# Kernel optimization log

Hardware: AMD Instinct MI355X
Metric: run time of the kernel (lower is better)

The kernel has to match this reference:

```python
import jax, jax.numpy as jnp
import numpy as np

B, N, D_V, D_H, D_K = 1024, 131072, 256, 256, 256


def setup_inputs() -> dict:
    key = jax.random.key(0)
    ks = jax.random.split(key, 12)
    s = 0.02
    V = jax.random.normal(ks[0], (B, D_V), dtype=jnp.float32)
    H = jax.random.normal(ks[1], (N, D_H), dtype=jnp.float32)
    batch_idx = jnp.sort(jax.random.randint(ks[2], (N,), 0, B)).astype(jnp.int32)
    Wq = jax.random.normal(ks[3], (D_K, D_V), dtype=jnp.float32) / np.sqrt(D_V)
    bq = jnp.zeros((D_K,), dtype=jnp.float32)
    Wk = jax.random.normal(ks[4], (D_K, D_H), dtype=jnp.float32) / np.sqrt(D_H)
    bk = jnp.zeros((D_K,), dtype=jnp.float32)
    Wv = jax.random.normal(ks[5], (D_V, D_H), dtype=jnp.float32) / np.sqrt(D_H)
    bv = jnp.zeros((D_V,), dtype=jnp.float32)
    Wo = jax.random.normal(ks[6], (D_V, 2 * D_V), dtype=jnp.float32) / np.sqrt(2 * D_V)
    bo = jnp.zeros((D_V,), dtype=jnp.float32)
    return {"V": V, "H": H, "batch_idx": batch_idx,
            "Wq": Wq, "bq": bq, "Wk": Wk, "bk": bk,
            "Wv": Wv, "bv": bv, "Wo": Wo, "bo": bo}


def reference(V, H, batch_idx, Wq, bq, Wk, bk, Wv, bv, Wo, bo):
    nb = V.shape[0]
    Q = V @ Wq.T + bq            # [B, d_k] one query per graph
    K = H @ Wk.T + bk            # [N, d_k]
    Vval = H @ Wv.T + bv         # [N, d_v]
    scale = 1.0 / jnp.sqrt(jnp.asarray(K.shape[-1], K.dtype))
    # ragged attention scores: each node attends to its graph's query
    scores = jnp.einsum('nd,nd->n', K, Q[batch_idx]) * scale   # [N]
    m = jax.ops.segment_max(scores, batch_idx, num_segments=nb)  # [B]
    e = jnp.exp(scores - m[batch_idx])
    denom = jax.ops.segment_sum(e, batch_idx, num_segments=nb)   # [B]
    attn = e / denom[batch_idx]                                  # [N]
    H_tilde = jax.ops.segment_sum(attn[:, None] * Vval, batch_idx, num_segments=nb)  # [B, d_v]
    U = jnp.concatenate([V, H_tilde], axis=-1)                   # [B, 2*d_v]
    out = U @ Wo.T + bo                                          # [B, d_v]
    # graphs with zero nodes pass V through unchanged
    count = jax.ops.segment_sum(jnp.ones_like(scores), batch_idx, num_segments=nb)
    return jnp.where((count > 0)[:, None], out, V)
```

## Files before the change

kernel.cpp:

```cpp
#include <hip/hip_runtime.h>
#include <math.h>

#define D 256
#define TWOD 512
#define BB 1024
#define NN 131072
#define LOG2E 1.4426950408889634f

typedef float v4f __attribute__((ext_vector_type(4)));

__device__ __forceinline__ v4f ldg_nt(const float* p, bool valid) {
  v4f z = {0.f, 0.f, 0.f, 0.f};
  if (valid) z = __builtin_nontemporal_load((const v4f*)p);
  return z;
}

__device__ __forceinline__ float dot4(v4f a, v4f b) {
  return fmaf(a.w, b.w, fmaf(a.z, b.z, fmaf(a.y, b.y, a.x * b.x)));
}

__device__ __forceinline__ float pack4(float d0, float d1, float d2, float d3) {
  float a01 = d0 + __shfl_xor(d1, 4);
  float a23 = d2 + __shfl_xor(d3, 4);
  float s = a01 + __shfl_xor(a23, 8);
  s += __shfl_xor(s, 1);
  s += __shfl_xor(s, 2);
  s += __shfl_xor(s, 16);
  s += __shfl_xor(s, 32);
  return s;
}

__global__ __launch_bounds__(256) void a_kernel(
    const float* __restrict__ V, const float* __restrict__ Wq,
    const float* __restrict__ Wk, const float* __restrict__ bq,
    const float* __restrict__ Wv, const float* __restrict__ Wo,
    const int* __restrict__ bidx,
    float* __restrict__ qt, float* __restrict__ WvT,
    float* __restrict__ WoT, int* __restrict__ offs) {
  __shared__ __align__(16) char smem[24576];
  const int blk = blockIdx.x;
  const int t = threadIdx.x;

  if (blk < 256) {
    float* Vs   = (float*)smem;
    float* q1s4 = (float*)(smem + 4096);
    float* part = (float*)(smem + 8192);
    const int wq = t >> 6, lane = t & 63;
    const int b0 = blk * 4;
    for (int i = 0; i < 4; ++i) Vs[i * 256 + t] = V[(size_t)(b0 + i) * D + t];
    __syncthreads();
    const int rot = (lane >> 2) & 3;
    const v4f vb0 = *(const v4f*)&Vs[0 * 256 + lane * 4];
    const v4f vb1 = *(const v4f*)&Vs[1 * 256 + lane * 4];
    const v4f vb2 = *(const v4f*)&Vs[2 * 256 + lane * 4];
    const v4f vb3 = *(const v4f*)&Vs[3 * 256 + lane * 4];

    for (int ii = 0; ii < 16; ++ii) {
      const int cb = wq * 64 + ii * 4;
      const v4f r0 = *(const v4f*)(Wq + (size_t)(cb + (rot ^ 0)) * D + lane * 4);
      const v4f r1 = *(const v4f*)(Wq + (size_t)(cb + (rot ^ 1)) * D + lane * 4);
      const v4f r2 = *(const v4f*)(Wq + (size_t)(cb + (rot ^ 2)) * D + lane * 4);
      const v4f r3 = *(const v4f*)(Wq + (size_t)(cb + (rot ^ 3)) * D + lane * 4);
      const float s0 = pack4(dot4(r0, vb0), dot4(r1, vb0), dot4(r2, vb0), dot4(r3, vb0));
      const float s1 = pack4(dot4(r0, vb1), dot4(r1, vb1), dot4(r2, vb1), dot4(r3, vb1));
      const float s2 = pack4(dot4(r0, vb2), dot4(r1, vb2), dot4(r2, vb2), dot4(r3, vb2));
      const float s3 = pack4(dot4(r0, vb3), dot4(r1, vb3), dot4(r2, vb3), dot4(r3, vb3));
      if (lane < 16 && (lane & 3) == 0) {
        v4f o = {s0, s1, s2, s3};
        *(v4f*)&q1s4[(cb + rot) * 4] = o;
      }
    }
    __syncthreads();

    v4f a0 = {0.f, 0.f, 0.f, 0.f}, a1 = a0, a2 = a0, a3 = a0;
    const int kb = wq * 64;
    for (int kk = 0; kk < 64; ++kk) {
      const int k = kb + kk;
      const v4f w4 = *(const v4f*)(Wk + (size_t)k * D + lane * 4);
      const v4f q = *(const v4f*)&q1s4[k * 4];
      const float bqk = bq[k];
      a0 += w4 * (q.x + bqk);
      a1 += w4 * (q.y + bqk);
      a2 += w4 * (q.z + bqk);
      a3 += w4 * (q.w + bqk);
    }
    *(v4f*)&part[(wq * 4 + 0) * 256 + lane * 4] = a0;
    *(v4f*)&part[(wq * 4 + 1) * 256 + lane * 4] = a1;
    *(v4f*)&part[(wq * 4 + 2) * 256 + lane * 4] = a2;
    *(v4f*)&part[(wq * 4 + 3) * 256 + lane * 4] = a3;
    __syncthreads();
    #pragma unroll
    for (int b = 0; b < 4; ++b) {
      const float s = part[(0 * 4 + b) * 256 + t] + part[(1 * 4 + b) * 256 + t] +
                      part[(2 * 4 + b) * 256 + t] + part[(3 * 4 + b) * 256 + t];
      qt[(size_t)(b0 + b) * D + t] = s;
    }
  } else if (blk < 304) {
    float (*tile)[65] = (float(*)[65])smem;
    const float* src; float* dst; int r0, c0, C;
    if (blk < 272) { int b = blk - 256; src = Wv; dst = WvT; C = 256; r0 = (b >> 2) * 64; c0 = (b & 3) * 64; }
    else           { int b = blk - 272; src = Wo; dst = WoT; C = 512; r0 = (b >> 3) * 64; c0 = (b & 7) * 64; }
    const int lane = t & 63, sr = t >> 6;
    #pragma unroll 4
    for (int rr = 0; rr < 16; ++rr) {
      const int r = rr * 4 + sr;
      tile[r][lane] = src[(size_t)(r0 + r) * C + c0 + lane];
    }
    __syncthreads();
    #pragma unroll 4
    for (int rr = 0; rr < 16; ++rr) {
      const int r = rr * 4 + sr;
      dst[(size_t)(c0 + r) * 256 + r0 + lane] = tile[lane][r];
    }
  } else {
    const int i = (blk - 304) * 256 + t;
    if (i >= NN) return;
    const int b1 = bidx[i];
    const int b2 = (i + 1 < NN) ? bidx[i + 1] : BB;
    if (i == 0) {
      for (int b = 0; b <= b1; ++b) offs[b] = 0;
    }
    for (int b = b1 + 1; b <= b2; ++b) offs[b] = i + 1;
  }
}

__global__ __launch_bounds__(1024) void f_kernel(
    const float* __restrict__ H, const float* __restrict__ qt,
    const int* __restrict__ offs, const float* __restrict__ V,
    const float* __restrict__ WvT, const float* __restrict__ WoT,
    const float* __restrict__ bv, const float* __restrict__ bo,
    float* __restrict__ out) {
  __shared__ __align__(16) float ss[16][D];
  __shared__ float sm[16], sd[16];
  __shared__ __align__(16) float sN2[D][4];
  __shared__ __align__(16) float Us2[TWOD][4];
  __shared__ __align__(16) float part[8][4][D];

  const int t = threadIdx.x;
  const int wave = t >> 6, lane = t & 63;
  const int blk = blockIdx.x;
  const int ib = wave >> 2, qq = wave & 3;
  const int bb = blk * 4 + ib;

  const int start = offs[bb], end = offs[bb + 1];
  const int cnt = end - start;
  const int step = (cnt + 3) >> 2;
  const int s0 = start + min(cnt, qq * step);
  const int e0 = start + min(cnt, (qq + 1) * step);

  float m = -1e30f, den = 0.f;
  v4f acc = {0.f, 0.f, 0.f, 0.f};

  if (s0 < e0) {
    const v4f q4 = *(const v4f*)(qt + (size_t)bb * D + lane * 4);
    const float SC = 0.0625f * LOG2E;
    const int odd = lane & 1;
    int n = s0;
    v4f c0 = ldg_nt(H + (size_t)n * D + lane * 4, true);
    v4f c1 = ldg_nt(H + (size_t)(n + 1) * D + lane * 4, n + 1 < e0);
    while (n < e0) {
      v4f p0 = ldg_nt(H + (size_t)(n + 2) * D + lane * 4, n + 2 < e0);
      v4f p1 = ldg_nt(H + (size_t)(n + 3) * D + lane * 4, n + 3 < e0);

      const float d0 = dot4(c0, q4);
      const float d1 = dot4(c1, q4);
      const float mine = odd ? d1 : d0;
      const float oth  = odd ? d0 : d1;
      float s = mine + __shfl_xor(oth, 1);
      s += __shfl_xor(s, 2);
      s += __shfl_xor(s, 4);
      s += __shfl_xor(s, 8);
      s += __shfl_xor(s, 16);
      s += __shfl_xor(s, 32);
      const float sc = (n + odd < e0) ? s * SC : -1e30f;

      const float mm = fmaxf(sc, __shfl_xor(sc, 1));
      const float nm = fmaxf(m, mm);
      const float f = exp2f(m - nm);
      const float w = exp2f(sc - nm);
      const float wx = __shfl_xor(w, 1);
      const float wr0 = odd ? wx : w;
      const float wr1 = odd ? w : wx;
      den = fmaf(den, f, w + wx);
      acc = acc * f + c0 * wr0 + c1 * wr1;
      m = nm;

      c0 = p0; c1 = p1; n += 2;
    }
  }
  *(v4f*)&ss[wave][lane * 4] = acc;
  if (lane == 0) { sm[wave] = m; sd[wave] = den; }
  __syncthreads();

  {
    const int i = t >> 8, d = t & 255;
    const int w0 = i * 4;
    const float m0 = sm[w0], m1 = sm[w0 + 1], m2 = sm[w0 + 2], m3 = sm[w0 + 3];
    const float M = fmaxf(fmaxf(m0, m1), fmaxf(m2, m3));
    const float f0 = exp2f(m0 - M), f1 = exp2f(m1 - M);
    const float f2 = exp2f(m2 - M), f3 = exp2f(m3 - M);
    const float Dn = sd[w0] * f0 + sd[w0 + 1] * f1 + sd[w0 + 2] * f2 + sd[w0 + 3] * f3;
    const float inv = (Dn > 0.f) ? (1.f / Dn) : 0.f;
    sN2[d][i] = (ss[w0][d] * f0 + ss[w0 + 1][d] * f1 +
                 ss[w0 + 2][d] * f2 + ss[w0 + 3][d] * f3) * inv;
    Us2[d][i] = V[(size_t)(blk * 4 + i) * D + d];
  }
  __syncthreads();

  v4f a0 = {0.f, 0.f, 0.f, 0.f}, a1 = a0, a2 = a0, a3 = a0;
  {
    const int hb = wave * 16;
    #pragma unroll 4
    for (int hh = 0; hh < 16; ++hh) {
      const int h = hb + hh;
      const v4f w4 = *(const v4f*)(WvT + (size_t)h * D + lane * 4);
      const v4f s4 = *(const v4f*)&sN2[h][0];
      a0 += w4 * s4.x; a1 += w4 * s4.y; a2 += w4 * s4.z; a3 += w4 * s4.w;
    }
  }
  if (wave >= 8) {
    *(v4f*)&part[wave - 8][0][lane * 4] = a0;
    *(v4f*)&part[wave - 8][1][lane * 4] = a1;
    *(v4f*)&part[wave - 8][2][lane * 4] = a2;
    *(v4f*)&part[wave - 8][3][lane * 4] = a3;
  }
  __syncthreads();
  if (wave < 8) {
    v4f p0 = *(const v4f*)&part[wave][0][lane * 4];
    v4f p1 = *(const v4f*)&part[wave][1][lane * 4];
    v4f p2 = *(const v4f*)&part[wave][2][lane * 4];
    v4f p3 = *(const v4f*)&part[wave][3][lane * 4];
    *(v4f*)&part[wave][0][lane * 4] = a0 + p0;
    *(v4f*)&part[wave][1][lane * 4] = a1 + p1;
    *(v4f*)&part[wave][2][lane * 4] = a2 + p2;
    *(v4f*)&part[wave][3][lane * 4] = a3 + p3;
  }
  __syncthreads();
  {
    const int i = t >> 8, d = t & 255;
    float s = bv[d];
    #pragma unroll
    for (int w = 0; w < 8; ++w) s += part[w][i][d];
    Us2[D + d][i] = s;
  }
  __syncthreads();

  a0 = (v4f){0.f, 0.f, 0.f, 0.f}; a1 = a0; a2 = a0; a3 = a0;
  {
    const int kb = wave * 32;
    #pragma unroll 4
    for (int kk = 0; kk < 32; ++kk) {
      const int k = kb + kk;
      const v4f w4 = *(const v4f*)(WoT + (size_t)k * D + lane * 4);
      const v4f u4 = *(const v4f*)&Us2[k][0];
      a0 += w4 * u4.x; a1 += w4 * u4.y; a2 += w4 * u4.z; a3 += w4 * u4.w;
    }
  }
  if (wave >= 8) {
    *(v4f*)&part[wave - 8][0][lane * 4] = a0;
    *(v4f*)&part[wave - 8][1][lane * 4] = a1;
    *(v4f*)&part[wave - 8][2][lane * 4] = a2;
    *(v4f*)&part[wave - 8][3][lane * 4] = a3;
  }
  __syncthreads();
  if (wave < 8) {
    v4f p0 = *(const v4f*)&part[wave][0][lane * 4];
    v4f p1 = *(const v4f*)&part[wave][1][lane * 4];
    v4f p2 = *(const v4f*)&part[wave][2][lane * 4];
    v4f p3 = *(const v4f*)&part[wave][3][lane * 4];
    *(v4f*)&part[wave][0][lane * 4] = a0 + p0;
    *(v4f*)&part[wave][1][lane * 4] = a1 + p1;
    *(v4f*)&part[wave][2][lane * 4] = a2 + p2;
    *(v4f*)&part[wave][3][lane * 4] = a3 + p3;
  }
  __syncthreads();
  {
    const int i = t >> 8, d = t & 255;
    const int bb2 = blk * 4 + i;
    float s = bo[d];
    #pragma unroll
    for (int w = 0; w < 8; ++w) s += part[w][i][d];
    const int c = offs[bb2 + 1] - offs[bb2];
    out[(size_t)bb2 * D + d] = (c > 0) ? s : Us2[d][i];
  }
}

extern "C" void kernel_launch(void* const* d_in, const int* in_sizes, int n_in,
                              void* d_out, int out_size, void* d_ws, size_t ws_size,
                              hipStream_t stream) {
  const float* V   = (const float*)d_in[0];
  const float* H   = (const float*)d_in[1];
  const int* bidx  = (const int*)d_in[2];
  const float* Wq  = (const float*)d_in[3];
  const float* bq  = (const float*)d_in[4];
  const float* Wk  = (const float*)d_in[5];
  const float* Wv  = (const float*)d_in[7];
  const float* bv  = (const float*)d_in[8];
  const float* Wo  = (const float*)d_in[9];
  const float* bo  = (const float*)d_in[10];
  float* out = (float*)d_out;

  float* ws  = (float*)d_ws;
  float* WvT = ws;
  float* WoT = WvT + D * D;
  float* qt  = WoT + TWOD * D;
  int* offs  = (int*)(qt + BB * D);

  hipLaunchKernelGGL(a_kernel, dim3(816), dim3(256), 0, stream,
                     V, Wq, Wk, bq, Wv, Wo, bidx, qt, WvT, WoT, offs);
  hipLaunchKernelGGL(f_kernel, dim3(BB / 4), dim3(1024), 0, stream,
                     H, qt, offs, V, WvT, WoT, bv, bo, out);
}
```

Measured before the change: 53.15 us.

## Fuse query projection into attention kernel and interleave node rows across waves

The Wq/Wk query-key projection moves out of the prologue kernel and into each attention block, so every block computes its own 4 folded query vectors in shared memory. This removes the qt global write and read and shrinks the first kernel to transposes plus offsets. Node rows are now interleaved across the four waves of a graph, in pairs with stride 8, rather than split into contiguous chunks. Shared memory is aliased between phases, which needs an extra barrier. In exchange, the f_kernel prologue is longer (it reads Wq and Wk per block), and that work now sits serially before the H streaming loop instead of in a separate kernel.

Measured after the change: 56.65 us. 1.07x slower.

```diff
diff --git a/kernel.cpp b/kernel.cpp
--- a/kernel.cpp
+++ b/kernel.cpp
@@ -30,33 +30,79 @@
   return s;
 }
 
-__global__ __launch_bounds__(256) void a_kernel(
-    const float* __restrict__ V, const float* __restrict__ Wq,
-    const float* __restrict__ Wk, const float* __restrict__ bq,
+__global__ __launch_bounds__(256) void t_kernel(
     const float* __restrict__ Wv, const float* __restrict__ Wo,
     const int* __restrict__ bidx,
-    float* __restrict__ qt, float* __restrict__ WvT,
-    float* __restrict__ WoT, int* __restrict__ offs) {
-  __shared__ __align__(16) char smem[24576];
+    float* __restrict__ WvT, float* __restrict__ WoT,
+    int* __restrict__ offs) {
   const int blk = blockIdx.x;
   const int t = threadIdx.x;
-
-  if (blk < 256) {
-    float* Vs   = (float*)smem;
-    float* q1s4 = (float*)(smem + 4096);
-    float* part = (float*)(smem + 8192);
-    const int wq = t >> 6, lane = t & 63;
-    const int b0 = blk * 4;
-    for (int i = 0; i < 4; ++i) Vs[i * 256 + t] = V[(size_t)(b0 + i) * D + t];
+  if (blk < 48) {
+    __shared__ float tile[64][65];
+    const float* src; float* dst; int r0, c0, C;
+    if (blk < 16) { src = Wv; dst = WvT; C = 256; r0 = (blk >> 2) * 64; c0 = (blk & 3) * 64; }
+    else          { int b = blk - 16; src = Wo; dst = WoT; C = 512; r0 = (b >> 3) * 64; c0 = (b & 7) * 64; }
+    const int lane = t & 63, sr = t >> 6;
+    #pragma unroll 4
+    for (int rr = 0; rr < 16; ++rr) {
+      const int r = rr * 4 + sr;
+      tile[r][lane] = src[(size_t)(r0 + r) * C + c0 + lane];
+    }
     __syncthreads();
+    #pragma unroll 4
+    for (int rr = 0; rr < 16; ++rr) {
+      const int r = rr * 4 + sr;
+      dst[(size_t)(c0 + r) * 256 + r0 + lane] = tile[lane][r];
+    }
+  } else {
+    const int i = (blk - 48) * 256 + t;
+    if (i >= NN) return;
+    const int b1 = bidx[i];
+    const int b2 = (i + 1 < NN) ? bidx[i + 1] : BB;
+    if (i == 0) {
+      for (int b = 0; b <= b1; ++b) offs[b] = 0;
+    }
+    for (int b = b1 + 1; b <= b2; ++b) offs[b] = i + 1;
+  }
+}
+
+__global__ __launch_bounds__(1024) void f_kernel(
+    const float* __restrict__ H, const float* __restrict__ V,
+    const float* __restrict__ Wq, const float* __restrict__ Wk,
+    const float* __restrict__ bq, const int* __restrict__ offs,
+    const float* __restrict__ WvT, const float* __restrict__ WoT,
+    const float* __restrict__ bv, const float* __restrict__ bo,
+    float* __restrict__ out) {
+  __shared__ __align__(16) char smem[61440];
+  float* partq = (float*)smem;
+  float (*ss)[D] = (float(*)[D])smem;
+  float* Vs   = (float*)(smem + 16384);
+  float* sN2  = (float*)(smem + 16384);
+  float* q1s4 = (float*)(smem + 20480);
+  float* Us2  = (float*)(smem + 20480);
+  float (*part)[4][D] = (float(*)[4][D])(smem + 28672);
+  __shared__ float sm[16], sd[16];
+
+  const int t = threadIdx.x;
+  const int wave = t >> 6, lane = t & 63;
+  const int blk = blockIdx.x;
+  const int b0 = blk * 4;
+
+  {
+    const int i = t >> 8, d = t & 255;
+    Vs[i * 256 + d] = V[(size_t)(b0 + i) * D + d];
+  }
+  __syncthreads();
+
+  {
     const int rot = (lane >> 2) & 3;
     const v4f vb0 = *(const v4f*)&Vs[0 * 256 + lane * 4];
     const v4f vb1 = *(const v4f*)&Vs[1 * 256 + lane * 4];
     const v4f vb2 = *(const v4f*)&Vs[2 * 256 + lane * 4];
     const v4f vb3 = *(const v4f*)&Vs[3 * 256 + lane * 4];
-
-    for (int ii = 0; ii < 16; ++ii) {
-      const int cb = wq * 64 + ii * 4;
+    #pragma unroll
+    for (int ii = 0; ii < 4; ++ii) {
+      const int cb = wave * 16 + ii * 4;
       const v4f r0 = *(const v4f*)(Wq + (size_t)(cb + (rot ^ 0)) * D + lane * 4);
       const v4f r1 = *(const v4f*)(Wq + (size_t)(cb + (rot ^ 1)) * D + lane * 4);
       const v4f r2 = *(const v4f*)(Wq + (size_t)(cb + (rot ^ 2)) * D + lane * 4);
@@ -70,97 +116,48 @@
         *(v4f*)&q1s4[(cb + rot) * 4] = o;
       }
     }
-    __syncthreads();
-
-    v4f a0 = {0.f, 0.f, 0.f, 0.f}, a1 = a0, a2 = a0, a3 = a0;
-    const int kb = wq * 64;
+  }
+  __syncthreads();
+
+  {
+    const int i = wave & 3, kq = wave >> 2;
+    v4f aq = {0.f, 0.f, 0.f, 0.f};
+    const int kb = kq * 64;
     for (int kk = 0; kk < 64; ++kk) {
       const int k = kb + kk;
       const v4f w4 = *(const v4f*)(Wk + (size_t)k * D + lane * 4);
-      const v4f q = *(const v4f*)&q1s4[k * 4];
-      const float bqk = bq[k];
-      a0 += w4 * (q.x + bqk);
-      a1 += w4 * (q.y + bqk);
-      a2 += w4 * (q.z + bqk);
-      a3 += w4 * (q.w + bqk);
-    }
-    *(v4f*)&part[(wq * 4 + 0) * 256 + lane * 4] = a0;
-    *(v4f*)&part[(wq * 4 + 1) * 256 + lane * 4] = a1;
-    *(v4f*)&part[(wq * 4 + 2) * 256 + lane * 4] = a2;
-    *(v4f*)&part[(wq * 4 + 3) * 256 + lane * 4] = a3;
-    __syncthreads();
-    #pragma unroll
-    for (int b = 0; b < 4; ++b) {
-      const float s = part[(0 * 4 + b) * 256 + t] + part[(1 * 4 + b) * 256 + t] +
-                      part[(2 * 4 + b) * 256 + t] + part[(3 * 4 + b) * 256 + t];
-      qt[(size_t)(b0 + b) * D + t] = s;
-    }
-  } else if (blk < 304) {
-    float (*tile)[65] = (float(*)[65])smem;
-    const float* src; float* dst; int r0, c0, C;
-    if (blk < 272) { int b = blk - 256; src = Wv; dst = WvT; C = 256; r0 = (b >> 2) * 64; c0 = (b & 3) * 64; }
-    else           { int b = blk - 272; src = Wo; dst = WoT; C = 512; r0 = (b >> 3) * 64; c0 = (b & 7) * 64; }
-    const int lane = t & 63, sr = t >> 6;
-    #pragma unroll 4
-    for (int rr = 0; rr < 16; ++rr) {
-      const int r = rr * 4 + sr;
-      tile[r][lane] = src[(size_t)(r0 + r) * C + c0 + lane];
-    }
-    __syncthreads();
-    #pragma unroll 4
-    for (int rr = 0; rr < 16; ++rr) {
-      const int r = rr * 4 + sr;
-      dst[(size_t)(c0 + r) * 256 + r0 + lane] = tile[lane][r];
-    }
-  } else {
-    const int i = (blk - 304) * 256 + t;
-    if (i >= NN) return;
-    const int b1 = bidx[i];
-    const int b2 = (i + 1 < NN) ? bidx[i + 1] : BB;
-    if (i == 0) {
-      for (int b = 0; b <= b1; ++b) offs[b] = 0;
-    }
-    for (int b = b1 + 1; b <= b2; ++b) offs[b] = i + 1;
-  }
-}
-
-__global__ __launch_bounds__(1024) void f_kernel(
-    const float* __restrict__ H, const float* __restrict__ qt,
-    const int* __restrict__ offs, const float* __restrict__ V,
-    const float* __restrict__ WvT, const float* __restrict__ WoT,
-    const float* __restrict__ bv, const float* __restrict__ bo,
-    float* __restrict__ out) {
-  __shared__ __align__(16) float ss[16][D];
-  __shared__ float sm[16], sd[16];
-  __shared__ __align__(16) float sN2[D][4];
-  __shared__ __align__(16) float Us2[TWOD][4];
-  __shared__ __align__(16) float part[8][4][D];
-
-  const int t = threadIdx.x;
-  const int wave = t >> 6, lane = t & 63;
-  const int blk = blockIdx.x;
+      aq += w4 * (q1s4[k * 4 + i] + bq[k]);
+    }
+    *(v4f*)&partq[(kq * 4 + i) * 256 + lane * 4] = aq;
+  }
+  __syncthreads();
+
   const int ib = wave >> 2, qq = wave & 3;
-  const int bb = blk * 4 + ib;
-
+  const int bb = b0 + ib;
   const int start = offs[bb], end = offs[bb + 1];
-  const int cnt = end - start;
-  const int step = (cnt + 3) >> 2;
-  const int s0 = start + min(cnt, qq * step);
-  const int e0 = start + min(cnt, (qq + 1) * step);
+
+  v4f q4;
+  {
+    const v4f p0 = *(const v4f*)&partq[(0 * 4 + ib) * 256 + lane * 4];
+    const v4f p1 = *(const v4f*)&partq[(1 * 4 + ib) * 256 + lane * 4];
+    const v4f p2 = *(const v4f*)&partq[(2 * 4 + ib) * 256 + lane * 4];
+    const v4f p3 = *(const v4f*)&partq[(3 * 4 + ib) * 256 + lane * 4];
+    q4 = (p0 + p1) + (p2 + p3);
+  }
+  __syncthreads();
 
   float m = -1e30f, den = 0.f;
   v4f acc = {0.f, 0.f, 0.f, 0.f};
-
-  if (s0 < e0) {
-    const v4f q4 = *(const v4f*)(qt + (size_t)bb * D + lane * 4);
+  {
     const float SC = 0.0625f * LOG2E;
     const int odd = lane & 1;
-    int n = s0;
-    v4f c0 = ldg_nt(H + (size_t)n * D + lane * 4, true);
-    v4f c1 = ldg_nt(H + (size_t)(n + 1) * D + lane * 4, n + 1 < e0);
-    while (n < e0) {
-      v4f p0 = ldg_nt(H + (size_t)(n + 2) * D + lane * 4, n + 2 < e0);
-      v4f p1 = ldg_nt(H + (size_t)(n + 3) * D + lane * 4, n + 3 < e0);
+    int n = start + qq * 2;
+    v4f c0 = ldg_nt(H + (size_t)n * D + lane * 4, n < end);
+    v4f c1 = ldg_nt(H + (size_t)(n + 1) * D + lane * 4, n + 1 < end);
+    while (n < end) {
+      const int nn = n + 8;
+      v4f p0 = ldg_nt(H + (size_t)nn * D + lane * 4, nn < end);
+      v4f p1 = ldg_nt(H + (size_t)(nn + 1) * D + lane * 4, nn + 1 < end);
 
       const float d0 = dot4(c0, q4);
       const float d1 = dot4(c1, q4);
@@ -172,7 +169,7 @@
       s += __shfl_xor(s, 8);
       s += __shfl_xor(s, 16);
       s += __shfl_xor(s, 32);
-      const float sc = (n + odd < e0) ? s * SC : -1e30f;
+      const float sc = (n + odd < end) ? s * SC : -1e30f;
 
       const float mm = fmaxf(sc, __shfl_xor(sc, 1));
       const float nm = fmaxf(m, mm);
@@ -185,7 +182,7 @@
       acc = acc * f + c0 * wr0 + c1 * wr1;
       m = nm;
 
-      c0 = p0; c1 = p1; n += 2;
+      c0 = p0; c1 = p1; n = nn;
     }
   }
   *(v4f*)&ss[wave][lane * 4] = acc;
@@ -201,9 +198,12 @@
     const float f2 = exp2f(m2 - M), f3 = exp2f(m3 - M);
     const float Dn = sd[w0] * f0 + sd[w0 + 1] * f1 + sd[w0 + 2] * f2 + sd[w0 + 3] * f3;
     const float inv = (Dn > 0.f) ? (1.f / Dn) : 0.f;
-    sN2[d][i] = (ss[w0][d] * f0 + ss[w0 + 1][d] * f1 +
-                 ss[w0 + 2][d] * f2 + ss[w0 + 3][d] * f3) * inv;
-    Us2[d][i] = V[(size_t)(blk * 4 + i) * D + d];
+    const float sv = (ss[w0][d] * f0 + ss[w0 + 1][d] * f1 +
+                      ss[w0 + 2][d] * f2 + ss[w0 + 3][d] * f3) * inv;
+    const float vv = V[(size_t)(b0 + i) * D + d];
+    __syncthreads();
+    sN2[d * 4 + i] = sv;
+    Us2[d * 4 + i] = vv;
   }
   __syncthreads();
 
@@ -214,7 +214,7 @@
     for (int hh = 0; hh < 16; ++hh) {
       const int h = hb + hh;
       const v4f w4 = *(const v4f*)(WvT + (size_t)h * D + lane * 4);
-      const v4f s4 = *(const v4f*)&sN2[h][0];
+      const v4f s4 = *(const v4f*)&sN2[h * 4];
       a0 += w4 * s4.x; a1 += w4 * s4.y; a2 += w4 * s4.z; a3 += w4 * s4.w;
     }
   }
@@ -241,7 +241,7 @@
     float s = bv[d];
     #pragma unroll
     for (int w = 0; w < 8; ++w) s += part[w][i][d];
-    Us2[D + d][i] = s;
+    Us2[(D + d) * 4 + i] = s;
   }
   __syncthreads();
 
@@ -252,7 +252,7 @@
     for (int kk = 0; kk < 32; ++kk) {
       const int k = kb + kk;
       const v4f w4 = *(const v4f*)(WoT + (size_t)k * D + lane * 4);
-      const v4f u4 = *(const v4f*)&Us2[k][0];
+      const v4f u4 = *(const v4f*)&Us2[k * 4];
       a0 += w4 * u4.x; a1 += w4 * u4.y; a2 += w4 * u4.z; a3 += w4 * u4.w;
     }
   }
@@ -276,12 +276,12 @@
   __syncthreads();
   {
     const int i = t >> 8, d = t & 255;
-    const int bb2 = blk * 4 + i;
+    const int bb2 = b0 + i;
     float s = bo[d];
     #pragma unroll
     for (int w = 0; w < 8; ++w) s += part[w][i][d];
     const int c = offs[bb2 + 1] - offs[bb2];
-    out[(size_t)bb2 * D + d] = (c > 0) ? s : Us2[d][i];
+    out[(size_t)bb2 * D + d] = (c > 0) ? s : Us2[d * 4 + i];
   }
 }
 
@@ -303,11 +303,10 @@
   float* ws  = (float*)d_ws;
   float* WvT = ws;
   float* WoT = WvT + D * D;
-  float* qt  = WoT + TWOD * D;
-  int* offs  = (int*)(qt + BB * D);
-
-  hipLaunchKernelGGL(a_kernel, dim3(816), dim3(256), 0, stream,
-                     V, Wq, Wk, bq, Wv, Wo, bidx, qt, WvT, WoT, offs);
+  int* offs  = (int*)(WoT + TWOD * D);
+
+  hipLaunchKernelGGL(t_kernel, dim3(560), dim3(256), 0, stream,
+                     Wv, Wo, bidx, WvT, WoT, offs);
   hipLaunchKernelGGL(f_kernel, dim3(BB / 4), dim3(1024), 0, stream,
-                     H, qt, offs, V, WvT, WoT, bv, bo, out);
-}
+                     H, V, Wq, Wk, bq, offs, WvT, WoT, bv, bo, out);
+}
```

## Fold Wv into Wo output projection and deepen H prefetch

Applied to the files above, without the earlier changes.

Precomputes a fused weight Wo[:,D:]·Wv and a combined bias cvec in the prep kernel, so the finalize stage runs one 512-wide matvec instead of two chained ones with their reductions and barriers. The streaming loop over H now prefetches two node pairs ahead instead of one, and per-graph offsets and V are staged in shared memory up front. Shared memory is aliased across phases to reduce the per-block footprint. The fused-weight computation adds serial 256-step loops to 64 prep blocks, which could lengthen the prep kernel.

Measured after the change: 54.07 us. No clear change (+1.7%).

```diff
diff --git a/kernel.cpp b/kernel.cpp
--- a/kernel.cpp
+++ b/kernel.cpp
@@ -30,13 +30,14 @@
   return s;
 }
 
-__global__ __launch_bounds__(256) void a_kernel(
+__global__ __launch_bounds__(256) void prep_kernel(
     const float* __restrict__ V, const float* __restrict__ Wq,
-    const float* __restrict__ Wk, const float* __restrict__ bq,
-    const float* __restrict__ Wv, const float* __restrict__ Wo,
+    const float* __restrict__ bq, const float* __restrict__ Wk,
+    const float* __restrict__ Wv, const float* __restrict__ bv,
+    const float* __restrict__ Wo, const float* __restrict__ bo,
     const int* __restrict__ bidx,
-    float* __restrict__ qt, float* __restrict__ WvT,
-    float* __restrict__ WoT, int* __restrict__ offs) {
+    float* __restrict__ qt, float* __restrict__ WfT,
+    float* __restrict__ cvec, int* __restrict__ offs) {
   __shared__ __align__(16) char smem[24576];
   const int blk = blockIdx.x;
   const int t = threadIdx.x;
@@ -95,25 +96,44 @@
                       part[(2 * 4 + b) * 256 + t] + part[(3 * 4 + b) * 256 + t];
       qt[(size_t)(b0 + b) * D + t] = s;
     }
-  } else if (blk < 304) {
+  } else if (blk < 320) {
+    const int h0 = (blk - 256) * 4;
+    float a0 = 0.f, a1 = 0.f, a2 = 0.f, a3 = 0.f;
+    for (int v = 0; v < D; ++v) {
+      const float wo = Wo[(size_t)t * TWOD + D + v];
+      const float* wvr = Wv + (size_t)v * D + h0;
+      a0 = fmaf(wvr[0], wo, a0);
+      a1 = fmaf(wvr[1], wo, a1);
+      a2 = fmaf(wvr[2], wo, a2);
+      a3 = fmaf(wvr[3], wo, a3);
+    }
+    WfT[(size_t)(D + h0 + 0) * D + t] = a0;
+    WfT[(size_t)(D + h0 + 1) * D + t] = a1;
+    WfT[(size_t)(D + h0 + 2) * D + t] = a2;
+    WfT[(size_t)(D + h0 + 3) * D + t] = a3;
+  } else if (blk < 336) {
     float (*tile)[65] = (float(*)[65])smem;
-    const float* src; float* dst; int r0, c0, C;
-    if (blk < 272) { int b = blk - 256; src = Wv; dst = WvT; C = 256; r0 = (b >> 2) * 64; c0 = (b & 3) * 64; }
-    else           { int b = blk - 272; src = Wo; dst = WoT; C = 512; r0 = (b >> 3) * 64; c0 = (b & 7) * 64; }
+    const int b = blk - 320;
+    const int r0 = (b >> 2) * 64, c0 = (b & 3) * 64;
     const int lane = t & 63, sr = t >> 6;
     #pragma unroll 4
     for (int rr = 0; rr < 16; ++rr) {
       const int r = rr * 4 + sr;
-      tile[r][lane] = src[(size_t)(r0 + r) * C + c0 + lane];
+      tile[r][lane] = Wo[(size_t)(r0 + r) * TWOD + c0 + lane];
     }
     __syncthreads();
     #pragma unroll 4
     for (int rr = 0; rr < 16; ++rr) {
       const int r = rr * 4 + sr;
-      dst[(size_t)(c0 + r) * 256 + r0 + lane] = tile[lane][r];
-    }
+      WfT[(size_t)(c0 + r) * D + r0 + lane] = tile[lane][r];
+    }
+  } else if (blk == 336) {
+    float a = bo[t];
+    for (int v = 0; v < D; ++v)
+      a = fmaf(Wo[(size_t)t * TWOD + D + v], bv[v], a);
+    cvec[t] = a;
   } else {
-    const int i = (blk - 304) * 256 + t;
+    const int i = (blk - 337) * 256 + t;
     if (i >= NN) return;
     const int b1 = bidx[i];
     const int b2 = (i + 1 < NN) ? bidx[i + 1] : BB;
@@ -125,42 +145,53 @@
 }
 
 __global__ __launch_bounds__(1024) void f_kernel(
-    const float* __restrict__ H, const float* __restrict__ qt,
-    const int* __restrict__ offs, const float* __restrict__ V,
-    const float* __restrict__ WvT, const float* __restrict__ WoT,
-    const float* __restrict__ bv, const float* __restrict__ bo,
+    const float* __restrict__ H, const float* __restrict__ V,
+    const float* __restrict__ qt, const int* __restrict__ offs,
+    const float* __restrict__ WfT, const float* __restrict__ cvec,
     float* __restrict__ out) {
-  __shared__ __align__(16) float ss[16][D];
+  __shared__ __align__(16) char smem[40960];
+  float (*ss)[D] = (float(*)[D])smem;
+  float (*part)[4][D] = (float(*)[4][D])smem;
+  float* Us2 = (float*)(smem + 32768);
   __shared__ float sm[16], sd[16];
-  __shared__ __align__(16) float sN2[D][4];
-  __shared__ __align__(16) float Us2[TWOD][4];
-  __shared__ __align__(16) float part[8][4][D];
+  __shared__ int soff[5];
 
   const int t = threadIdx.x;
   const int wave = t >> 6, lane = t & 63;
   const int blk = blockIdx.x;
-  const int ib = wave >> 2, qq = wave & 3;
-  const int bb = blk * 4 + ib;
-
-  const int start = offs[bb], end = offs[bb + 1];
-  const int cnt = end - start;
-  const int step = (cnt + 3) >> 2;
-  const int s0 = start + min(cnt, qq * step);
-  const int e0 = start + min(cnt, (qq + 1) * step);
+  const int b0 = blk * 4;
+
+  if (t < 5) soff[t] = offs[b0 + t];
+  {
+    const int i = t >> 8, d = t & 255;
+    Us2[d * 4 + i] = V[(size_t)(b0 + i) * D + d];
+  }
+  __syncthreads();
+
+  const int ib = wave >> 2, ph = wave & 3;
+  const int bb = b0 + ib;
+  const int start = soff[ib];
+  const int cnt = soff[ib + 1] - start;
+  const int ck = (cnt + 3) >> 2;
+  const int s0 = start + min(cnt, ph * ck);
+  const int e0 = start + min(cnt, (ph + 1) * ck);
+
+  const v4f q4 = *(const v4f*)(qt + (size_t)bb * D + lane * 4);
+  int n = s0;
+  v4f c0 = ldg_nt(H + (size_t)n * D + lane * 4, n < e0);
+  v4f c1 = ldg_nt(H + (size_t)(n + 1) * D + lane * 4, n + 1 < e0);
+  v4f f0 = ldg_nt(H + (size_t)(n + 2) * D + lane * 4, n + 2 < e0);
+  v4f f1 = ldg_nt(H + (size_t)(n + 3) * D + lane * 4, n + 3 < e0);
 
   float m = -1e30f, den = 0.f;
   v4f acc = {0.f, 0.f, 0.f, 0.f};
-
-  if (s0 < e0) {
-    const v4f q4 = *(const v4f*)(qt + (size_t)bb * D + lane * 4);
+  {
     const float SC = 0.0625f * LOG2E;
     const int odd = lane & 1;
-    int n = s0;
-    v4f c0 = ldg_nt(H + (size_t)n * D + lane * 4, true);
-    v4f c1 = ldg_nt(H + (size_t)(n + 1) * D + lane * 4, n + 1 < e0);
     while (n < e0) {
-      v4f p0 = ldg_nt(H + (size_t)(n + 2) * D + lane * 4, n + 2 < e0);
-      v4f p1 = ldg_nt(H + (size_t)(n + 3) * D + lane * 4, n + 3 < e0);
+      const int nn = n + 4;
+      v4f g0 = ldg_nt(H + (size_t)nn * D + lane * 4, nn < e0);
+      v4f g1 = ldg_nt(H + (size_t)(nn + 1) * D + lane * 4, nn + 1 < e0);
 
       const float d0 = dot4(c0, q4);
       const float d1 = dot4(c1, q4);
@@ -185,7 +216,7 @@
       acc = acc * f + c0 * wr0 + c1 * wr1;
       m = nm;
 
-      c0 = p0; c1 = p1; n += 2;
+      c0 = f0; c1 = f1; f0 = g0; f1 = g1; n += 2;
     }
   }
   *(v4f*)&ss[wave][lane * 4] = acc;
@@ -197,91 +228,54 @@
     const int w0 = i * 4;
     const float m0 = sm[w0], m1 = sm[w0 + 1], m2 = sm[w0 + 2], m3 = sm[w0 + 3];
     const float M = fmaxf(fmaxf(m0, m1), fmaxf(m2, m3));
-    const float f0 = exp2f(m0 - M), f1 = exp2f(m1 - M);
-    const float f2 = exp2f(m2 - M), f3 = exp2f(m3 - M);
-    const float Dn = sd[w0] * f0 + sd[w0 + 1] * f1 + sd[w0 + 2] * f2 + sd[w0 + 3] * f3;
+    const float f0m = exp2f(m0 - M), f1m = exp2f(m1 - M);
+    const float f2m = exp2f(m2 - M), f3m = exp2f(m3 - M);
+    const float Dn = sd[w0] * f0m + sd[w0 + 1] * f1m + sd[w0 + 2] * f2m + sd[w0 + 3] * f3m;
     const float inv = (Dn > 0.f) ? (1.f / Dn) : 0.f;
-    sN2[d][i] = (ss[w0][d] * f0 + ss[w0 + 1][d] * f1 +
-                 ss[w0 + 2][d] * f2 + ss[w0 + 3][d] * f3) * inv;
-    Us2[d][i] = V[(size_t)(blk * 4 + i) * D + d];
+    const float sv = (ss[w0][d] * f0m + ss[w0 + 1][d] * f1m +
+                      ss[w0 + 2][d] * f2m + ss[w0 + 3][d] * f3m) * inv;
+    __syncthreads();
+    Us2[(D + d) * 4 + i] = sv;
   }
   __syncthreads();
 
-  v4f a0 = {0.f, 0.f, 0.f, 0.f}, a1 = a0, a2 = a0, a3 = a0;
-  {
-    const int hb = wave * 16;
-    #pragma unroll 4
-    for (int hh = 0; hh < 16; ++hh) {
-      const int h = hb + hh;
-      const v4f w4 = *(const v4f*)(WvT + (size_t)h * D + lane * 4);
-      const v4f s4 = *(const v4f*)&sN2[h][0];
-      a0 += w4 * s4.x; a1 += w4 * s4.y; a2 += w4 * s4.z; a3 += w4 * s4.w;
-    }
-  }
-  if (wave >= 8) {
-    *(v4f*)&part[wave - 8][0][lane * 4] = a0;
-    *(v4f*)&part[wave - 8][1][lane * 4] = a1;
-    *(v4f*)&part[wave - 8][2][lane * 4] = a2;
-    *(v4f*)&part[wave - 8][3][lane * 4] = a3;
-  }
-  __syncthreads();
-  if (wave < 8) {
-    v4f p0 = *(const v4f*)&part[wave][0][lane * 4];
-    v4f p1 = *(const v4f*)&part[wave][1][lane * 4];
-    v4f p2 = *(const v4f*)&part[wave][2][lane * 4];
-    v4f p3 = *(const v4f*)&part[wave][3][lane * 4];
-    *(v4f*)&part[wave][0][lane * 4] = a0 + p0;
-    *(v4f*)&part[wave][1][lane * 4] = a1 + p1;
-    *(v4f*)&part[wave][2][lane * 4] = a2 + p2;
-    *(v4f*)&part[wave][3][lane * 4] = a3 + p3;
-  }
-  __syncthreads();
-  {
-    const int i = t >> 8, d = t & 255;
-    float s = bv[d];
-    #pragma unroll
-    for (int w = 0; w < 8; ++w) s += part[w][i][d];
-    Us2[D + d][i] = s;
-  }
-  __syncthreads();
-
-  a0 = (v4f){0.f, 0.f, 0.f, 0.f}; a1 = a0; a2 = a0; a3 = a0;
-  {
+  {
+    v4f a0 = {0.f, 0.f, 0.f, 0.f}, a1 = a0, a2 = a0, a3 = a0;
     const int kb = wave * 32;
     #pragma unroll 4
     for (int kk = 0; kk < 32; ++kk) {
       const int k = kb + kk;
-      const v4f w4 = *(const v4f*)(WoT + (size_t)k * D + lane * 4);
-      const v4f u4 = *(const v4f*)&Us2[k][0];
+      const v4f w4 = *(const v4f*)(WfT + (size_t)k * D + lane * 4);
+      const v4f u4 = *(const v4f*)&Us2[k * 4];
       a0 += w4 * u4.x; a1 += w4 * u4.y; a2 += w4 * u4.z; a3 += w4 * u4.w;
     }
-  }
-  if (wave >= 8) {
-    *(v4f*)&part[wave - 8][0][lane * 4] = a0;
-    *(v4f*)&part[wave - 8][1][lane * 4] = a1;
-    *(v4f*)&part[wave - 8][2][lane * 4] = a2;
-    *(v4f*)&part[wave - 8][3][lane * 4] = a3;
+    if (wave >= 8) {
+      *(v4f*)&part[wave - 8][0][lane * 4] = a0;
+      *(v4f*)&part[wave - 8][1][lane * 4] = a1;
+      *(v4f*)&part[wave - 8][2][lane * 4] = a2;
+      *(v4f*)&part[wave - 8][3][lane * 4] = a3;
+    }
+    __syncthreads();
+    if (wave < 8) {
+      v4f p0 = *(const v4f*)&part[wave][0][lane * 4];
+      v4f p1 = *(const v4f*)&part[wave][1][lane * 4];
+      v4f p2 = *(const v4f*)&part[wave][2][lane * 4];
+      v4f p3 = *(const v4f*)&part[wave][3][lane * 4];
+      *(v4f*)&part[wave][0][lane * 4] = a0 + p0;
+      *(v4f*)&part[wave][1][lane * 4] = a1 + p1;
+      *(v4f*)&part[wave][2][lane * 4] = a2 + p2;
+      *(v4f*)&part[wave][3][lane * 4] = a3 + p3;
+    }
   }
   __syncthreads();
-  if (wave < 8) {
-    v4f p0 = *(const v4f*)&part[wave][0][lane * 4];
-    v4f p1 = *(const v4f*)&part[wave][1][lane * 4];
-    v4f p2 = *(const v4f*)&part[wave][2][lane * 4];
-    v4f p3 = *(const v4f*)&part[wave][3][lane * 4];
-    *(v4f*)&part[wave][0][lane * 4] = a0 + p0;
-    *(v4f*)&part[wave][1][lane * 4] = a1 + p1;
-    *(v4f*)&part[wave][2][lane * 4] = a2 + p2;
-    *(v4f*)&part[wave][3][lane * 4] = a3 + p3;
-  }
-  __syncthreads();
   {
     const int i = t >> 8, d = t & 255;
-    const int bb2 = blk * 4 + i;
-    float s = bo[d];
+    const int bb2 = b0 + i;
+    float s = cvec[d];
     #pragma unroll
     for (int w = 0; w < 8; ++w) s += part[w][i][d];
-    const int c = offs[bb2 + 1] - offs[bb2];
-    out[(size_t)bb2 * D + d] = (c > 0) ? s : Us2[d][i];
+    const int c = soff[i + 1] - soff[i];
+    out[(size_t)bb2 * D + d] = (c > 0) ? s : Us2[d * 4 + i];
   }
 }
 
@@ -301,13 +295,14 @@
   float* out = (float*)d_out;
 
   float* ws  = (float*)d_ws;
-  float* WvT = ws;
-  float* WoT = WvT + D * D;
-  float* qt  = WoT + TWOD * D;
-  int* offs  = (int*)(qt + BB * D);
-
-  hipLaunchKernelGGL(a_kernel, dim3(816), dim3(256), 0, stream,
-                     V, Wq, Wk, bq, Wv, Wo, bidx, qt, WvT, WoT, offs);
+  float* qtb = ws;
+  float* WfT = qtb + BB * D;
+  float* cv  = WfT + TWOD * D;
+  int* offs  = (int*)(cv + D);
+
+  hipLaunchKernelGGL(prep_kernel, dim3(849), dim3(256), 0, stream,
+                     V, Wq, bq, Wk, Wv, bv, Wo, bo, bidx,
+                     qtb, WfT, cv, offs);
   hipLaunchKernelGGL(f_kernel, dim3(BB / 4), dim3(1024), 0, stream,
-                     H, qt, offs, V, WvT, WoT, bv, bo, out);
-}
+                     H, V, qtb, offs, WfT, cv, out);
+}
```
